# Optimization experiments

Measured on AMD Instinct MI355X. Metric: run time of the kernel, lower is better.

The kernel has to match this reference:

```python
import jax, jax.numpy as jnp
import numpy as np
import math

N, E, G = 20000, 160000, 256
H, L, R, LAT, TD = 128, 4, 64, 128, 64
CUT = 6.0
NTYPES = 101  # max_atomic_num=100 -> 101 rows, row 0 is padding


def _lin(key, fan_in, fan_out):
    kw, _ = jax.random.split(key)
    w = jax.random.normal(kw, (fan_in, fan_out), jnp.float32) / np.sqrt(fan_in).astype(np.float32)
    b = jnp.zeros((fan_out,), jnp.float32)
    return w, b


def _stack_lin(key, fan_in, fan_out):
    keys = jax.random.split(key, L)
    ws, bs = zip(*[_lin(k, fan_in, fan_out) for k in keys])
    return jnp.stack(ws), jnp.stack(bs)


def setup_inputs() -> dict:
    key = jax.random.key(0)
    ks = list(jax.random.split(key, 24))
    noisy_coords = jax.random.uniform(ks[0], (N, 3), jnp.float32)
    noisy_types = jax.random.randint(ks[1], (N,), 0, NTYPES)
    z = jax.random.normal(ks[2], (G, LAT), jnp.float32)
    t = jax.random.uniform(ks[3], (G,), jnp.float32) * 1000.0
    edge_index = jax.random.randint(ks[4], (2, E), 0, N)
    batch = jnp.sort(jax.random.randint(ks[5], (N,), 0, G))
    lattice = jnp.eye(3, dtype=jnp.float32)[None] * 5.0 + 0.1 * jax.random.normal(ks[6], (G, 3, 3), jnp.float32)
    offsets = jax.random.randint(ks[7], (E, 3), -1, 2).astype(jnp.float32)
    atom_embed = jax.random.normal(ks[8], (NTYPES, H), jnp.float32) * 0.02
    atom_embed = atom_embed.at[0].set(0.0)  # padding_idx=0
    z_w, z_b = _lin(ks[9], LAT, H)
    t_w, t_b = _lin(ks[10], TD, H)
    msg_w1, msg_b1 = _stack_lin(ks[11], H, H)
    msg_w2, msg_b2 = _stack_lin(ks[12], H, 3 * H)
    rbf_w, rbf_b = _stack_lin(ks[13], R, 3 * H)
    U = jax.random.normal(ks[14], (L, H, H), jnp.float32) / np.sqrt(H).astype(np.float32)
    V = jax.random.normal(ks[15], (L, H, H), jnp.float32) / np.sqrt(H).astype(np.float32)
    upd_w1, upd_b1 = _stack_lin(ks[16], 2 * H, H)
    upd_w2, upd_b2 = _stack_lin(ks[17], H, 3 * H)
    hc_w1, hc_b1 = _lin(ks[18], H, H)
    hc_w2, hc_b2 = _lin(ks[19], H, 3)
    ht_w1, ht_b1 = _lin(ks[20], H, H)
    ht_w2, ht_b2 = _lin(ks[21], H, NTYPES)
    return dict(noisy_coords=noisy_coords, noisy_types=noisy_types, z=z, t=t,
                edge_index=edge_index, batch=batch, lattice=lattice, offsets=offsets,
                atom_embed=atom_embed, z_w=z_w, z_b=z_b, t_w=t_w, t_b=t_b,
                msg_w1=msg_w1, msg_b1=msg_b1, msg_w2=msg_w2, msg_b2=msg_b2,
                rbf_w=rbf_w, rbf_b=rbf_b, U=U, V=V,
                upd_w1=upd_w1, upd_b1=upd_b1, upd_w2=upd_w2, upd_b2=upd_b2,
                hc_w1=hc_w1, hc_b1=hc_b1, hc_w2=hc_w2, hc_b2=hc_b2,
                ht_w1=ht_w1, ht_b1=ht_b1, ht_w2=ht_w2, ht_b2=ht_b2)


def reference(noisy_coords, noisy_types, z, t, edge_index, batch, lattice, offsets,
              atom_embed, z_w, z_b, t_w, t_b,
              msg_w1, msg_b1, msg_w2, msg_b2, rbf_w, rbf_b, U, V,
              upd_w1, upd_b1, upd_w2, upd_b2,
              hc_w1, hc_b1, hc_w2, hc_b2, ht_w1, ht_b1, ht_w2, ht_b2):
    n = noisy_coords.shape[0]
    src, dst = edge_index[0], edge_index[1]

    # node embeddings + conditioning
    s = atom_embed[noisy_types]                       # [N, H]
    v = jnp.zeros((n, 3, H), s.dtype)                 # [N, 3, H]
    half = TD // 2
    freqs = jnp.exp(-math.log(10000.0) * jnp.arange(half, dtype=jnp.float32) / (half - 1))
    emb = t[:, None] * freqs[None, :]                 # [G, TD/2]
    t_emb = jnp.concatenate([jnp.sin(emb), jnp.cos(emb)], axis=-1)  # [G, TD]
    cond = (z @ z_w + z_b)[batch] + (t_emb @ t_w + t_b)[batch]      # [N, H]

    # edge geometry: gather -> diff -> 3x3 matmul -> norm -> RBF -> normalize
    frac_diff = noisy_coords[dst] - noisy_coords[src] + offsets     # [E, 3]
    cart = jnp.einsum('ei,eij->ej', frac_diff, lattice[batch[src]]) # [E, 3]
    dist = jnp.maximum(jnp.sqrt(jnp.sum(cart * cart, -1)), 1e-8)    # clamp(min=1e-8)
    centers = jnp.linspace(0.0, CUT, R)
    gamma = jnp.float32(R / CUT)
    rbf = jnp.exp(-gamma * (dist[:, None] - centers[None, :]) ** 2) # [E, R]
    unit = cart / jnp.maximum(jnp.sqrt(jnp.sum(cart * cart, -1, keepdims=True)), 1e-12)

    # PaiNN layers (canonical message + update blocks)
    for l in range(L):
        s = s + cond
        # message block
        phi = jax.nn.silu(s @ msg_w1[l] + msg_b1[l]) @ msg_w2[l] + msg_b2[l]  # [N, 3H]
        filt = rbf @ rbf_w[l] + rbf_b[l]                                      # [E, 3H]
        x = phi[src] * filt
        ds, dv1, dv2 = jnp.split(x, 3, axis=-1)
        s = s + jax.ops.segment_sum(ds, dst, num_segments=n)
        vmsg = dv1[:, None, :] * v[src] + dv2[:, None, :] * unit[:, :, None]  # [E, 3, H]
        v = v + jax.ops.segment_sum(vmsg, dst, num_segments=n)
        # update block
        Uv = jnp.einsum('nch,hk->nck', v, U[l])
        Vv = jnp.einsum('nch,hk->nck', v, V[l])
        Vn = jnp.sqrt(jnp.sum(Vv * Vv, axis=1) + 1e-8)                        # [N, H]
        a = jax.nn.silu(jnp.concatenate([s, Vn], -1) @ upd_w1[l] + upd_b1[l]) @ upd_w2[l] + upd_b2[l]
        avv, asv, ass = jnp.split(a, 3, axis=-1)
        v = v + avv[:, None, :] * Uv
        s = s + asv * jnp.sum(Uv * Vv, axis=1) + ass

    coords_out = jax.nn.silu(s @ hc_w1 + hc_b1) @ hc_w2 + hc_b2   # [N, 3]
    type_out = jax.nn.silu(s @ ht_w1 + ht_b1) @ ht_w2 + ht_b2     # [N, 101]
    return coords_out, type_out
```

## Files before the change

kernel.cpp:

```cpp
#include <hip/hip_runtime.h>
#include <hip/hip_bf16.h>

#define HD 128
#define RD 64
#define H3 384

typedef float f32x4 __attribute__((ext_vector_type(4)));
typedef unsigned short us8 __attribute__((ext_vector_type(8)));
typedef __bf16 bf16x8 __attribute__((ext_vector_type(8)));

__device__ __forceinline__ float silu_f(float x) {
    return x / (1.0f + __expf(-x));
}
__device__ __forceinline__ unsigned short f2bf(float x) {
    __hip_bfloat16 h = __float2bfloat16(x);
    return *reinterpret_cast<unsigned short*>(&h);
}
__device__ __forceinline__ float bf2f(unsigned short u) {
    return __uint_as_float(((unsigned)u) << 16);
}
__device__ __forceinline__ f32x4 mfma3(us8 ah, us8 al, us8 bh, us8 bl, f32x4 c) {
    bf16x8 AH = __builtin_bit_cast(bf16x8, ah);
    bf16x8 AL = __builtin_bit_cast(bf16x8, al);
    bf16x8 BH = __builtin_bit_cast(bf16x8, bh);
    bf16x8 BL = __builtin_bit_cast(bf16x8, bl);
    c = __builtin_amdgcn_mfma_f32_16x16x32_bf16(AH, BH, c, 0, 0, 0);
    c = __builtin_amdgcn_mfma_f32_16x16x32_bf16(AH, BL, c, 0, 0, 0);
    c = __builtin_amdgcn_mfma_f32_16x16x32_bf16(AL, BH, c, 0, 0, 0);
    return c;
}

__global__ void wprep_kernel(const float* __restrict__ src,
                             unsigned short* __restrict__ dhi, unsigned short* __restrict__ dlo,
                             int K, int OUT, int sStride, int dStride, int nlay) {
    int total = K * OUT;
    for (int idx = blockIdx.x * blockDim.x + threadIdx.x; idx < total * nlay;
         idx += gridDim.x * blockDim.x) {
        int lyr = idx / total, r = idx % total;
        int o = r / K, k = r % K;
        float x = src[(size_t)lyr * sStride + (size_t)k * OUT + o];
        unsigned short hi = f2bf(x);
        unsigned short lo = f2bf(x - bf2f(hi));
        dhi[(size_t)lyr * dStride + (size_t)o * K + k] = hi;
        dlo[(size_t)lyr * dStride + (size_t)o * K + k] = lo;
    }
}

__global__ __launch_bounds__(128) void cond_kernel(const float* __restrict__ z, const float* __restrict__ t,
                            const float* __restrict__ z_w, const float* __restrict__ z_b,
                            const float* __restrict__ t_w, const float* __restrict__ t_b,
                            float* __restrict__ condG) {
    int g = blockIdx.x;
    int k = threadIdx.x;
    __shared__ float zr[128];
    __shared__ float te[64];
    zr[k] = z[g * 128 + k];
    if (k < 32) {
        float f = __expf(-9.2103403719761836f * (float)k / 31.0f);
        float e = t[g] * f;
        te[k] = sinf(e);
        te[32 + k] = cosf(e);
    }
    __syncthreads();
    float acc = z_b[k] + t_b[k];
    #pragma unroll 8
    for (int i = 0; i < 128; ++i) acc += zr[i] * z_w[i * 128 + k];
    #pragma unroll 8
    for (int i = 0; i < 64; ++i) acc += te[i] * t_w[i * 128 + k];
    condG[g * 128 + k] = acc;
}

__global__ void init_kernel(const int* __restrict__ types, const float* __restrict__ emb,
                            const float* __restrict__ condG, const int* __restrict__ batch,
                            float* __restrict__ s, int N_) {
    int i = blockIdx.x * blockDim.x + threadIdx.x;
    if (i < N_ * HD) {
        int n = i >> 7;
        int k = i & 127;
        s[i] = emb[types[n] * HD + k] + condG[batch[n] * 128 + k];
    }
}

__global__ void geom_kernel(const float* __restrict__ coords, const int* __restrict__ srcI,
                            const int* __restrict__ dstI, const int* __restrict__ batch,
                            const float* __restrict__ lattice, const float* __restrict__ offs,
                            float* __restrict__ dist, float* __restrict__ unit, int E_) {
    int e = blockIdx.x * blockDim.x + threadIdx.x;
    if (e >= E_) return;
    int sn = srcI[e], dn = dstI[e];
    float f0 = coords[dn * 3 + 0] - coords[sn * 3 + 0] + offs[e * 3 + 0];
    float f1 = coords[dn * 3 + 1] - coords[sn * 3 + 1] + offs[e * 3 + 1];
    float f2 = coords[dn * 3 + 2] - coords[sn * 3 + 2] + offs[e * 3 + 2];
    const float* Lg = lattice + batch[sn] * 9;
    float c0 = f0 * Lg[0] + f1 * Lg[3] + f2 * Lg[6];
    float c1 = f0 * Lg[1] + f1 * Lg[4] + f2 * Lg[7];
    float c2 = f0 * Lg[2] + f1 * Lg[5] + f2 * Lg[8];
    float nrm = sqrtf(c0 * c0 + c1 * c1 + c2 * c2);
    dist[e] = fmaxf(nrm, 1e-8f);
    float inv = 1.0f / fmaxf(nrm, 1e-12f);
    unit[e * 3 + 0] = c0 * inv;
    unit[e * 3 + 1] = c1 * inv;
    unit[e * 3 + 2] = c2 * inv;
}

__global__ void hist_kernel(const int* __restrict__ dstI, int* __restrict__ cnt, int E_) {
    int e = blockIdx.x * blockDim.x + threadIdx.x;
    if (e < E_) atomicAdd(&cnt[dstI[e]], 1);
}

__global__ __launch_bounds__(1024) void scan_kernel(const int* __restrict__ cnt, int* __restrict__ cur, int n) {
    __shared__ int tmp[1024];
    __shared__ int carry_s;
    if (threadIdx.x == 0) carry_s = 0;
    __syncthreads();
    for (int base = 0; base < n; base += 1024) {
        int i = base + threadIdx.x;
        int x = (i < n) ? cnt[i] : 0;
        tmp[threadIdx.x] = x;
        __syncthreads();
        for (int off = 1; off < 1024; off <<= 1) {
            int y = (threadIdx.x >= off) ? tmp[threadIdx.x - off] : 0;
            __syncthreads();
            tmp[threadIdx.x] += y;
            __syncthreads();
        }
        if (i < n) cur[i] = carry_s + tmp[threadIdx.x] - x;
        __syncthreads();
        if (threadIdx.x == 0) carry_s += tmp[1023];
        __syncthreads();
    }
}

__global__ void scatter_kernel(const int* __restrict__ srcI, const int* __restrict__ dstI,
                               const float* __restrict__ dist, const float* __restrict__ unit,
                               int* __restrict__ cur,
                               float* __restrict__ dist_s, float* __restrict__ unit_s,
                               int* __restrict__ src_s, int* __restrict__ dst_s, int E_) {
    int e = blockIdx.x * blockDim.x + threadIdx.x;
    if (e >= E_) return;
    int d = dstI[e];
    int p = atomicAdd(&cur[d], 1);
    dist_s[p] = dist[e];
    unit_s[p * 3 + 0] = unit[e * 3 + 0];
    unit_s[p * 3 + 1] = unit[e * 3 + 1];
    unit_s[p * 3 + 2] = unit[e * 3 + 2];
    src_s[p] = srcI[e];
    dst_s[p] = d;
}

#define PSA 136
__global__ __launch_bounds__(256, 2) void phi_mfma(
    const float* __restrict__ s,
    const unsigned short* __restrict__ w1h, const unsigned short* __restrict__ w1l,
    const float* __restrict__ b1,
    const unsigned short* __restrict__ w2h, const unsigned short* __restrict__ w2l,
    const float* __restrict__ b2,
    float* __restrict__ phi, int N_) {
    __shared__ unsigned short Ah[32 * PSA], Al[32 * PSA], Hh[32 * PSA], Hl[32 * PSA];
    const int tid = threadIdx.x;
    const int n0 = blockIdx.x * 32;
    for (int idx = tid; idx < 32 * 128; idx += 256) {
        int j = idx >> 7, k = idx & 127;
        int n = n0 + j; if (n >= N_) n = N_ - 1;
        float x = s[(size_t)n * 128 + k];
        unsigned short h = f2bf(x);
        Ah[j * PSA + k] = h;
        Al[j * PSA + k] = f2bf(x - bf2f(h));
    }
    __syncthreads();
    const int w = tid >> 6, l = tid & 63;
    const int lr = l & 15, lk = (l >> 4) << 3, rg0 = (l >> 4) << 2;
    const f32x4 zero4 = {0.0f, 0.0f, 0.0f, 0.0f};
    f32x4 acc1[2][2];
    #pragma unroll
    for (int rt = 0; rt < 2; ++rt)
        #pragma unroll
        for (int ci = 0; ci < 2; ++ci) acc1[rt][ci] = zero4;
    #pragma unroll
    for (int kt = 0; kt < 4; ++kt) {
        int kk = kt * 32 + lk;
        us8 bh[2], bl[2], ah[2], alo[2];
        #pragma unroll
        for (int ci = 0; ci < 2; ++ci) {
            int col = (w * 2 + ci) * 16 + lr;
            bh[ci] = *(const us8*)(w1h + (size_t)col * 128 + kk);
            bl[ci] = *(const us8*)(w1l + (size_t)col * 128 + kk);
        }
        #pragma unroll
        for (int rt = 0; rt < 2; ++rt) {
            ah[rt]  = *(const us8*)(Ah + (rt * 16 + lr) * PSA + kk);
            alo[rt] = *(const us8*)(Al + (rt * 16 + lr) * PSA + kk);
        }
        #pragma unroll
        for (int rt = 0; rt < 2; ++rt)
            #pragma unroll
            for (int ci = 0; ci < 2; ++ci)
                acc1[rt][ci] = mfma3(ah[rt], alo[rt], bh[ci], bl[ci], acc1[rt][ci]);
    }
    #pragma unroll
    for (int rt = 0; rt < 2; ++rt)
        #pragma unroll
        for (int ci = 0; ci < 2; ++ci) {
            int col = (w * 2 + ci) * 16 + lr;
            float bb = b1[col];
            #pragma unroll
            for (int rg = 0; rg < 4; ++rg) {
                int j = rt * 16 + rg0 + rg;
                float hv = silu_f(acc1[rt][ci][rg] + bb);
                unsigned short hh = f2bf(hv);
                Hh[j * PSA + col] = hh;
                Hl[j * PSA + col] = f2bf(hv - bf2f(hh));
            }
        }
    __syncthreads();
    f32x4 acc2[2][6];
    #pragma unroll
    for (int rt = 0; rt < 2; ++rt)
        #pragma unroll
        for (int ci = 0; ci < 6; ++ci) acc2[rt][ci] = zero4;
    #pragma unroll
    for (int kt = 0; kt < 4; ++kt) {
        int kk = kt * 32 + lk;
        us8 ah[2], alo[2];
        #pragma unroll
        for (int rt = 0; rt < 2; ++rt) {
            ah[rt]  = *(const us8*)(Hh + (rt * 16 + lr) * PSA + kk);
            alo[rt] = *(const us8*)(Hl + (rt * 16 + lr) * PSA + kk);
        }
        #pragma unroll
        for (int ci = 0; ci < 6; ++ci) {
            int col = (w * 6 + ci) * 16 + lr;
            us8 bh = *(const us8*)(w2h + (size_t)col * 128 + kk);
            us8 bl = *(const us8*)(w2l + (size_t)col * 128 + kk);
            #pragma unroll
            for (int rt = 0; rt < 2; ++rt)
                acc2[rt][ci] = mfma3(ah[rt], alo[rt], bh, bl, acc2[rt][ci]);
        }
    }
    #pragma unroll
    for (int rt = 0; rt < 2; ++rt)
        #pragma unroll
        for (int ci = 0; ci < 6; ++ci) {
            int col = (w * 6 + ci) * 16 + lr;
            float bb = b2[col];
            #pragma unroll
            for (int rg = 0; rg < 4; ++rg) {
                int j = rt * 16 + rg0 + rg;
                int n = n0 + j;
                if (n < N_) phi[(size_t)n * 384 + col] = acc2[rt][ci][rg] + bb;
            }
        }
}

__global__ __launch_bounds__(256, 2) void upd_mfma(
    const unsigned short* __restrict__ Uh, const unsigned short* __restrict__ Ul,
    const unsigned short* __restrict__ Vh, const unsigned short* __restrict__ Vl,
    const unsigned short* __restrict__ w1h, const unsigned short* __restrict__ w1l,
    const float* __restrict__ b1,
    const unsigned short* __restrict__ w2h, const unsigned short* __restrict__ w2l,
    const float* __restrict__ b2,
    float* __restrict__ s, float* __restrict__ v, const float* __restrict__ dv,
    const float* __restrict__ condG, const int* __restrict__ batch, int addcond, int N_) {
    __shared__ unsigned short SMA[2 * 48 * 136];
    __shared__ float UvL[48 * 132];
    __shared__ float VvL[48 * 132];
    unsigned short* VNh = SMA;
    unsigned short* VNl = SMA + 48 * 136;
    unsigned short* A1h = SMA;
    unsigned short* A1l = SMA + 16 * 264;
    unsigned short* a1h = SMA + 32 * 264;
    unsigned short* a1l = SMA + 32 * 264 + 16 * 136;
    float* o384 = VvL;
    const int tid = threadIdx.x;
    const int n0 = blockIdx.x * 16;
    for (int idx = tid; idx < 48 * 128; idx += 256) {
        int r = idx >> 7, k = idx & 127;
        int c = r >> 4, j = r & 15;
        int n = n0 + j; if (n >= N_) n = N_ - 1;
        size_t off = (size_t)n * 384 + c * 128 + k;
        float x = v[off] + dv[off];
        unsigned short h = f2bf(x);
        VNh[r * 136 + k] = h;
        VNl[r * 136 + k] = f2bf(x - bf2f(h));
    }
    __syncthreads();
    const int w = tid >> 6, l = tid & 63;
    const int lr = l & 15, lk = (l >> 4) << 3, rg0 = (l >> 4) << 2;
    const f32x4 zero4 = {0.0f, 0.0f, 0.0f, 0.0f};
    {
        f32x4 acc[3][2];
        #pragma unroll
        for (int rt = 0; rt < 3; ++rt) { acc[rt][0] = zero4; acc[rt][1] = zero4; }
        #pragma unroll
        for (int kt = 0; kt < 4; ++kt) {
            int kk = kt * 32 + lk;
            us8 bh[2], bl[2];
            #pragma unroll
            for (int ci = 0; ci < 2; ++ci) {
                int col = (w * 2 + ci) * 16 + lr;
                bh[ci] = *(const us8*)(Uh + (size_t)col * 128 + kk);
                bl[ci] = *(const us8*)(Ul + (size_t)col * 128 + kk);
            }
            #pragma unroll
            for (int rt = 0; rt < 3; ++rt) {
                us8 ah  = *(const us8*)(VNh + (rt * 16 + lr) * 136 + kk);
                us8 alo = *(const us8*)(VNl + (rt * 16 + lr) * 136 + kk);
                #pragma unroll
                for (int ci = 0; ci < 2; ++ci)
                    acc[rt][ci] = mfma3(ah, alo, bh[ci], bl[ci], acc[rt][ci]);
            }
        }
        #pragma unroll
        for (int rt = 0; rt < 3; ++rt)
            #pragma unroll
            for (int ci = 0; ci < 2; ++ci) {
                int col = (w * 2 + ci) * 16 + lr;
                #pragma unroll
                for (int rg = 0; rg < 4; ++rg)
                    UvL[(rt * 16 + rg0 + rg) * 132 + col] = acc[rt][ci][rg];
            }
        #pragma unroll
        for (int rt = 0; rt < 3; ++rt) { acc[rt][0] = zero4; acc[rt][1] = zero4; }
        #pragma unroll
        for (int kt = 0; kt < 4; ++kt) {
            int kk = kt * 32 + lk;
            us8 bh[2], bl[2];
            #pragma unroll
            for (int ci = 0; ci < 2; ++ci) {
                int col = (w * 2 + ci) * 16 + lr;
                bh[ci] = *(const us8*)(Vh + (size_t)col * 128 + kk);
                bl[ci] = *(const us8*)(Vl + (size_t)col * 128 + kk);
            }
            #pragma unroll
            for (int rt = 0; rt < 3; ++rt) {
                us8 ah  = *(const us8*)(VNh + (rt * 16 + lr) * 136 + kk);
                us8 alo = *(const us8*)(VNl + (rt * 16 + lr) * 136 + kk);
                #pragma unroll
                for (int ci = 0; ci < 2; ++ci)
                    acc[rt][ci] = mfma3(ah, alo, bh[ci], bl[ci], acc[rt][ci]);
            }
        }
        #pragma unroll
        for (int rt = 0; rt < 3; ++rt)
            #pragma unroll
            for (int ci = 0; ci < 2; ++ci) {
                int col = (w * 2 + ci) * 16 + lr;
                #pragma unroll
                for (int rg = 0; rg < 4; ++rg)
                    VvL[(rt * 16 + rg0 + rg) * 132 + col] = acc[rt][ci][rg];
            }
    }
    __syncthreads();
    float dotr[8];
    {
        int k = tid & 127;
        int jb = (tid >> 7) * 8;
        #pragma unroll
        for (int i = 0; i < 8; ++i) {
            int j = jb + i;
            float uv0 = UvL[j * 132 + k], uv1 = UvL[(16 + j) * 132 + k], uv2 = UvL[(32 + j) * 132 + k];
            float vv0 = VvL[j * 132 + k], vv1 = VvL[(16 + j) * 132 + k], vv2 = VvL[(32 + j) * 132 + k];
            dotr[i] = uv0 * vv0 + uv1 * vv1 + uv2 * vv2;
            float vnv = sqrtf(vv0 * vv0 + vv1 * vv1 + vv2 * vv2 + 1e-8f);
            int n = n0 + j; if (n >= N_) n = N_ - 1;
            float sv = s[(size_t)n * 128 + k];
            unsigned short h1 = f2bf(sv);
            A1h[j * 264 + k] = h1;
            A1l[j * 264 + k] = f2bf(sv - bf2f(h1));
            unsigned short h2 = f2bf(vnv);
            A1h[j * 264 + 128 + k] = h2;
            A1l[j * 264 + 128 + k] = f2bf(vnv - bf2f(h2));
        }
    }
    __syncthreads();
    {
        f32x4 acc[2]; acc[0] = zero4; acc[1] = zero4;
        #pragma unroll
        for (int kt = 0; kt < 8; ++kt) {
            int kk = kt * 32 + lk;
            us8 ah  = *(const us8*)(A1h + lr * 264 + kk);
            us8 alo = *(const us8*)(A1l + lr * 264 + kk);
            #pragma unroll
            for (int ci = 0; ci < 2; ++ci) {
                int col = (w * 2 + ci) * 16 + lr;
                us8 bh = *(const us8*)(w1h + (size_t)col * 256 + kk);
                us8 bl = *(const us8*)(w1l + (size_t)col * 256 + kk);
                acc[ci] = mfma3(ah, alo, bh, bl, acc[ci]);
            }
        }
        #pragma unroll
        for (int ci = 0; ci < 2; ++ci) {
            int col = (w * 2 + ci) * 16 + lr;
            float bb = b1[col];
            #pragma unroll
            for (int rg = 0; rg < 4; ++rg) {
                int j = rg0 + rg;
                float hv = silu_f(acc[ci][rg] + bb);
                unsigned short hh = f2bf(hv);
                a1h[j * 136 + col] = hh;
                a1l[j * 136 + col] = f2bf(hv - bf2f(hh));
            }
        }
    }
    __syncthreads();
    {
        f32x4 acc[6];
        #pragma unroll
        for (int ci = 0; ci < 6; ++ci) acc[ci] = zero4;
        #pragma unroll
        for (int kt = 0; kt < 4; ++kt) {
            int kk = kt * 32 + lk;
            us8 ah  = *(const us8*)(a1h + lr * 136 + kk);
            us8 alo = *(const us8*)(a1l + lr * 136 + kk);
            #pragma unroll
            for (int ci = 0; ci < 6; ++ci) {
                int col = (w * 6 + ci) * 16 + lr;
                us8 bh = *(const us8*)(w2h + (size_t)col * 128 + kk);
                us8 bl = *(const us8*)(w2l + (size_t)col * 128 + kk);
                acc[ci] = mfma3(ah, alo, bh, bl, acc[ci]);
            }
        }
        #pragma unroll
        for (int ci = 0; ci < 6; ++ci) {
            int col = (w * 6 + ci) * 16 + lr;
            float bb = b2[col];
            #pragma unroll
            for (int rg = 0; rg < 4; ++rg) {
                int j = rg0 + rg;
                o384[j * 388 + col] = acc[ci][rg] + bb;
            }
        }
    }
    __syncthreads();
    {
        int k = tid & 127;
        int jb = (tid >> 7) * 8;
        #pragma unroll
        for (int i = 0; i < 8; ++i) {
            int j = jb + i;
            int n = n0 + j;
            if (n >= N_) continue;
            float a0  = o384[j * 388 + k];
            float aH  = o384[j * 388 + 128 + k];
            float a2v = o384[j * 388 + 256 + k];
            #pragma unroll
            for (int c = 0; c < 3; ++c) {
                size_t off = (size_t)n * 384 + c * 128 + k;
                v[off] = v[off] + dv[off] + a0 * UvL[(c * 16 + j) * 132 + k];
            }
            float cadd = addcond ? condG[(size_t)batch[n] * 128 + k] : 0.0f;
            s[(size_t)n * 128 + k] += aH * dotr[i] + a2v + cadd;
        }
    }
}

#define EPB 128
__global__ __launch_bounds__(512) void edge_kernel(
    const float* __restrict__ phi, const float* __restrict__ v,
    const float* __restrict__ dist_s, const float* __restrict__ unit_s,
    const int* __restrict__ src_s, const int* __restrict__ dst_s,
    const float* __restrict__ rw, const float* __restrict__ rb,
    float* __restrict__ s, float* __restrict__ dv, int E_) {
    __shared__ unsigned short w_lds[RD * H3];
    __shared__ float rbf_lds[4][4][RD];
    for (int i = threadIdx.x; i < RD * H3; i += 512) {
        w_lds[i] = f2bf(rw[i]);
    }
    int sub = threadIdx.x >> 7;
    int col = threadIdx.x & 127;
    float b0 = rb[col], b1 = rb[128 + col], b2 = rb[256 + col];
    int span0 = blockIdx.x * EPB + sub * 32;
    float as = 0.0f, ad0 = 0.0f, ad1 = 0.0f, ad2 = 0.0f;
    int rd = -1;
    for (int it = 0; it < 8; ++it) {
        int eb = span0 + it * 4;
        __syncthreads();
        {
            int r = col & 63;
            int jbase = col >> 6;
            #pragma unroll
            for (int jj = 0; jj < 2; ++jj) {
                int j = jbase + 2 * jj;
                int e = eb + j;
                float val = 0.0f;
                if (e < E_) {
                    float d = dist_s[e];
                    float c = 6.0f * (float)r / 63.0f;
                    float tt = d - c;
                    val = __expf(-(64.0f / 6.0f) * tt * tt);
                }
                rbf_lds[sub][j][r] = val;
            }
        }
        __syncthreads();
        float f[4][3] = {};
        #pragma unroll 4
        for (int r = 0; r < 64; ++r) {
            float w0 = bf2f(w_lds[r * 384 + col]);
            float w1 = bf2f(w_lds[r * 384 + 128 + col]);
            float w2 = bf2f(w_lds[r * 384 + 256 + col]);
            #pragma unroll
            for (int j = 0; j < 4; ++j) {
                float rbv = rbf_lds[sub][j][r];
                f[j][0] += rbv * w0;
                f[j][1] += rbv * w1;
                f[j][2] += rbv * w2;
            }
        }
        #pragma unroll
        for (int j = 0; j < 4; ++j) {
            int e = eb + j;
            if (e >= E_) break;
            int dn = dst_s[e];
            if (dn != rd) {
                if (rd >= 0) {
                    atomicAdd(&s[(size_t)rd * 128 + col], as);
                    atomicAdd(&dv[(size_t)rd * 384 + col], ad0);
                    atomicAdd(&dv[(size_t)rd * 384 + 128 + col], ad1);
                    atomicAdd(&dv[(size_t)rd * 384 + 256 + col], ad2);
                }
                as = ad0 = ad1 = ad2 = 0.0f;
                rd = dn;
            }
            int sn = src_s[e];
            const float* phr = phi + (size_t)sn * 384;
            const float* vr = v + (size_t)sn * 384;
            float x0 = phr[col] * (f[j][0] + b0);
            float x1 = phr[128 + col] * (f[j][1] + b1);
            float x2 = phr[256 + col] * (f[j][2] + b2);
            float u0 = unit_s[e * 3 + 0], u1 = unit_s[e * 3 + 1], u2 = unit_s[e * 3 + 2];
            as += x0;
            ad0 += x1 * vr[col] + x2 * u0;
            ad1 += x1 * vr[128 + col] + x2 * u1;
            ad2 += x1 * vr[256 + col] + x2 * u2;
        }
    }
    if (rd >= 0) {
        atomicAdd(&s[(size_t)rd * 128 + col], as);
        atomicAdd(&dv[(size_t)rd * 384 + col], ad0);
        atomicAdd(&dv[(size_t)rd * 384 + 128 + col], ad1);
        atomicAdd(&dv[(size_t)rd * 384 + 256 + col], ad2);
    }
}

#define HPB 8
__global__ __launch_bounds__(128, 4) void heads_kernel(
    const float* __restrict__ s,
    const float* __restrict__ hc_w1, const float* __restrict__ hc_b1,
    const float* __restrict__ hc_w2, const float* __restrict__ hc_b2,
    const float* __restrict__ ht_w1, const float* __restrict__ ht_b1,
    const float* __restrict__ ht_w2, const float* __restrict__ ht_b2,
    float* __restrict__ outc, float* __restrict__ outt, int N_) {
    int n0 = blockIdx.x * HPB;
    int k = threadIdx.x;
    __shared__ float sr[HPB][128];
    __shared__ float h1[HPB][128];
    __shared__ float h2[HPB][128];
    #pragma unroll
    for (int j = 0; j < HPB; ++j) {
        int n = n0 + j;
        sr[j][k] = (n < N_) ? s[(size_t)n * 128 + k] : 0.0f;
    }
    __syncthreads();
    float a[HPB], b[HPB];
    #pragma unroll
    for (int j = 0; j < HPB; ++j) { a[j] = hc_b1[k]; b[j] = ht_b1[k]; }
    for (int h = 0; h < 128; h += 4) {
        float wa0 = hc_w1[h * 128 + k],       wa1 = hc_w1[(h + 1) * 128 + k];
        float wa2 = hc_w1[(h + 2) * 128 + k], wa3 = hc_w1[(h + 3) * 128 + k];
        float wb0 = ht_w1[h * 128 + k],       wb1 = ht_w1[(h + 1) * 128 + k];
        float wb2 = ht_w1[(h + 2) * 128 + k], wb3 = ht_w1[(h + 3) * 128 + k];
        #pragma unroll
        for (int j = 0; j < HPB; ++j) {
            const float4 x = *reinterpret_cast<const float4*>(&sr[j][h]);
            a[j] = fmaf(x.w, wa3, fmaf(x.z, wa2, fmaf(x.y, wa1, fmaf(x.x, wa0, a[j]))));
            b[j] = fmaf(x.w, wb3, fmaf(x.z, wb2, fmaf(x.y, wb1, fmaf(x.x, wb0, b[j]))));
        }
    }
    #pragma unroll
    for (int j = 0; j < HPB; ++j) {
        h1[j][k] = silu_f(a[j]);
        h2[j][k] = silu_f(b[j]);
    }
    __syncthreads();
    if (k < 101) {
        for (int j = 0; j < HPB; ++j) {
            int n = n0 + j;
            if (n >= N_) break;
            float c = ht_b2[k];
            #pragma unroll 4
            for (int h = 0; h < 128; ++h) c += h2[j][h] * ht_w2[h * 101 + k];
            outt[(size_t)n * 101 + k] = c;
        }
    }
    if (k < 3) {
        for (int j = 0; j < HPB; ++j) {
            int n = n0 + j;
            if (n >= N_) break;
            float c = hc_b2[k];
            #pragma unroll 4
            for (int h = 0; h < 128; ++h) c += h1[j][h] * hc_w2[h * 3 + k];
            outc[(size_t)n * 3 + k] = c;
        }
    }
}

extern "C" void kernel_launch(void* const* d_in, const int* in_sizes, int n_in,
                              void* d_out, int out_size, void* d_ws, size_t ws_size,
                              hipStream_t stream) {
    const float* coords  = (const float*)d_in[0];
    const int*   types   = (const int*)d_in[1];
    const float* z       = (const float*)d_in[2];
    const float* t       = (const float*)d_in[3];
    const int*   eidx    = (const int*)d_in[4];
    const int*   batch   = (const int*)d_in[5];
    const float* lattice = (const float*)d_in[6];
    const float* offs    = (const float*)d_in[7];
    const float* aemb    = (const float*)d_in[8];
    const float* z_w     = (const float*)d_in[9];
    const float* z_b     = (const float*)d_in[10];
    const float* t_w     = (const float*)d_in[11];
    const float* t_b     = (const float*)d_in[12];
    const float* msg_w1  = (const float*)d_in[13];
    const float* msg_b1  = (const float*)d_in[14];
    const float* msg_w2  = (const float*)d_in[15];
    const float* msg_b2  = (const float*)d_in[16];
    const float* rbf_w   = (const float*)d_in[17];
    const float* rbf_b   = (const float*)d_in[18];
    const float* Um      = (const float*)d_in[19];
    const float* Vm      = (const float*)d_in[20];
    const float* upd_w1  = (const float*)d_in[21];
    const float* upd_b1  = (const float*)d_in[22];
    const float* upd_w2  = (const float*)d_in[23];
    const float* upd_b2  = (const float*)d_in[24];
    const float* hc_w1   = (const float*)d_in[25];
    const float* hc_b1   = (const float*)d_in[26];
    const float* hc_w2   = (const float*)d_in[27];
    const float* hc_b2   = (const float*)d_in[28];
    const float* ht_w1   = (const float*)d_in[29];
    const float* ht_b1   = (const float*)d_in[30];
    const float* ht_w2   = (const float*)d_in[31];
    const float* ht_b2   = (const float*)d_in[32];

    const int N = in_sizes[1];
    const int G = in_sizes[3];
    const int E = in_sizes[4] / 2;
    const int* srcI = eidx;
    const int* dstI = eidx + E;

    char* ws = (char*)d_ws;
    auto alloc = [&](size_t bytes) {
        char* p = ws;
        ws += (bytes + 255) & ~(size_t)255;
        return p;
    };
    float* s_buf   = (float*)alloc((size_t)N * HD * 4);
    float* v_buf   = (float*)alloc((size_t)N * H3 * 4);
    float* dv_buf  = (float*)alloc((size_t)N * H3 * 4);
    float* phi_buf = (float*)alloc((size_t)N * H3 * 4);
    float* condG   = (float*)alloc((size_t)G * HD * 4);
    float* dist_s  = (float*)alloc((size_t)E * 4);
    float* unit_s  = (float*)alloc((size_t)E * 3 * 4);
    int*   src_s   = (int*)alloc((size_t)E * 4);
    int*   dst_s   = (int*)alloc((size_t)E * 4);
    int*   cur     = (int*)alloc((size_t)N * 4);
    unsigned short* wpr = (unsigned short*)alloc((size_t)4 * 360448 * 2);
    const size_t LS = 360448;
    float* dist_t  = phi_buf;
    float* unit_t  = phi_buf + E;

    hipMemsetAsync(v_buf, 0, (size_t)N * H3 * 4, stream);
    hipMemsetAsync(cur, 0, (size_t)N * 4, stream);
    cond_kernel<<<G, 128, 0, stream>>>(z, t, z_w, z_b, t_w, t_b, condG);
    init_kernel<<<(N * HD + 255) / 256, 256, 0, stream>>>(types, aemb, condG, batch, s_buf, N);
    geom_kernel<<<(E + 255) / 256, 256, 0, stream>>>(coords, srcI, dstI, batch, lattice, offs, dist_t, unit_t, E);
    hist_kernel<<<(E + 255) / 256, 256, 0, stream>>>(dstI, cur, E);
    {
        int* cnt2 = (int*)(phi_buf + 4 * (size_t)E);
        hipMemcpyAsync(cnt2, cur, (size_t)N * 4, hipMemcpyDeviceToDevice, stream);
        scan_kernel<<<1, 1024, 0, stream>>>(cnt2, cur, N);
    }
    scatter_kernel<<<(E + 255) / 256, 256, 0, stream>>>(srcI, dstI, dist_t, unit_t, cur,
                                                        dist_s, unit_s, src_s, dst_s, E);
    wprep_kernel<<<256, 256, 0, stream>>>(msg_w1, wpr + 0,      wpr + 16384,  128, 128, 16384, (int)LS, 4);
    wprep_kernel<<<768, 256, 0, stream>>>(msg_w2, wpr + 32768,  wpr + 81920,  128, 384, 49152, (int)LS, 4);
    wprep_kernel<<<512, 256, 0, stream>>>(upd_w1, wpr + 131072, wpr + 163840, 256, 128, 32768, (int)LS, 4);
    wprep_kernel<<<768, 256, 0, stream>>>(upd_w2, wpr + 196608, wpr + 245760, 128, 384, 49152, (int)LS, 4);
    wprep_kernel<<<256, 256, 0, stream>>>(Um,     wpr + 294912, wpr + 311296, 128, 128, 16384, (int)LS, 4);
    wprep_kernel<<<256, 256, 0, stream>>>(Vm,     wpr + 327680, wpr + 344064, 128, 128, 16384, (int)LS, 4);

    int eblocks = (E + EPB - 1) / EPB;
    int pblocks = (N + 31) / 32;
    int ublocks = (N + 15) / 16;
    int hblocks = (N + HPB - 1) / HPB;
    for (int l = 0; l < 4; ++l) {
        const unsigned short* L = wpr + (size_t)l * LS;
        phi_mfma<<<pblocks, 256, 0, stream>>>(s_buf,
                L + 0, L + 16384, msg_b1 + (size_t)l * HD,
                L + 32768, L + 81920, msg_b2 + (size_t)l * H3,
                phi_buf, N);
        hipMemsetAsync(dv_buf, 0, (size_t)N * H3 * 4, stream);
        edge_kernel<<<eblocks, 512, 0, stream>>>(phi_buf, v_buf, dist_s, unit_s, src_s, dst_s,
                                                 rbf_w + (size_t)l * RD * H3, rbf_b + (size_t)l * H3,
                                                 s_buf, dv_buf, E);
        upd_mfma<<<ublocks, 256, 0, stream>>>(
                L + 294912, L + 311296, L + 327680, L + 344064,
                L + 131072, L + 163840, upd_b1 + (size_t)l * HD,
                L + 196608, L + 245760, upd_b2 + (size_t)l * H3,
                s_buf, v_buf, dv_buf, condG, batch, (l < 3) ? 1 : 0, N);
    }
    heads_kernel<<<hblocks, 128, 0, stream>>>(s_buf, hc_w1, hc_b1, hc_w2, hc_b2,
                                        ht_w1, ht_b1, ht_w2, ht_b2,
                                        (float*)d_out, (float*)d_out + (size_t)N * 3, N);
}
```

Baseline: 1.465 ms.

## Compute edge RBF filter with split-bf16 MFMA using prepacked weights

Replaces the scalar FMA loop that computed the per-edge RBF filter (64x384 weights held as bf16 in LDS) with split-bf16 (hi/lo) MFMA tiles over 64-edge blocks. The filter is staged through LDS for the existing scatter/atomic accumulation. The RBF weights are now pre-split into hi/lo bf16 once per launch by wprep, which removes the per-block conversion of the 24K-element weight matrix into LDS. The new kernel uses 256-thread blocks with a large LDS footprint (about 68KB), which may limit occupancy. It also halves edges per block, so more atomic flushes happen at block boundaries.

```diff
diff --git a/kernel.cpp b/kernel.cpp
--- a/kernel.cpp
+++ b/kernel.cpp
@@ -454,62 +454,84 @@
     }
 }
 
-#define EPB 128
-__global__ __launch_bounds__(512) void edge_kernel(
+#define EB 64
+__global__ __launch_bounds__(256, 2) void edge_mfma(
     const float* __restrict__ phi, const float* __restrict__ v,
     const float* __restrict__ dist_s, const float* __restrict__ unit_s,
     const int* __restrict__ src_s, const int* __restrict__ dst_s,
-    const float* __restrict__ rw, const float* __restrict__ rb,
+    const unsigned short* __restrict__ rwh, const unsigned short* __restrict__ rwl,
+    const float* __restrict__ rb,
     float* __restrict__ s, float* __restrict__ dv, int E_) {
-    __shared__ unsigned short w_lds[RD * H3];
-    __shared__ float rbf_lds[4][4][RD];
-    for (int i = threadIdx.x; i < RD * H3; i += 512) {
-        w_lds[i] = f2bf(rw[i]);
-    }
-    int sub = threadIdx.x >> 7;
-    int col = threadIdx.x & 127;
+    __shared__ unsigned short Rh[64 * 72];
+    __shared__ unsigned short Rl[64 * 72];
+    __shared__ float filt[32 * 388];
+    const int tid = threadIdx.x;
+    const int e0 = blockIdx.x * EB;
+    #pragma unroll
+    for (int i = 0; i < 16; ++i) {
+        int idx = i * 256 + tid;
+        int e = idx >> 6, r = idx & 63;
+        float val = 0.0f;
+        int ge = e0 + e;
+        if (ge < E_) {
+            float d = dist_s[ge];
+            float c = 6.0f * (float)r / 63.0f;
+            float tt = d - c;
+            val = __expf(-(64.0f / 6.0f) * tt * tt);
+        }
+        unsigned short h = f2bf(val);
+        Rh[e * 72 + r] = h;
+        Rl[e * 72 + r] = f2bf(val - bf2f(h));
+    }
+    __syncthreads();
+    const int w = tid >> 6, l = tid & 63;
+    const int lr = l & 15, lk = (l >> 4) << 3, rg0 = (l >> 4) << 2;
+    const f32x4 zero4 = {0.0f, 0.0f, 0.0f, 0.0f};
+    f32x4 acc[4][6];
+    #pragma unroll
+    for (int mt = 0; mt < 4; ++mt)
+        #pragma unroll
+        for (int nt = 0; nt < 6; ++nt) acc[mt][nt] = zero4;
+    #pragma unroll
+    for (int kt = 0; kt < 2; ++kt) {
+        int kk = kt * 32 + lk;
+        us8 ah[4], al[4];
+        #pragma unroll
+        for (int mt = 0; mt < 4; ++mt) {
+            ah[mt] = *(const us8*)(Rh + (mt * 16 + lr) * 72 + kk);
+            al[mt] = *(const us8*)(Rl + (mt * 16 + lr) * 72 + kk);
+        }
+        #pragma unroll
+        for (int nt = 0; nt < 6; ++nt) {
+            int col = w * 96 + nt * 16 + lr;
+            us8 bh = *(const us8*)(rwh + (size_t)col * 64 + kk);
+            us8 bl = *(const us8*)(rwl + (size_t)col * 64 + kk);
+            #pragma unroll
+            for (int mt = 0; mt < 4; ++mt)
+                acc[mt][nt] = mfma3(ah[mt], al[mt], bh, bl, acc[mt][nt]);
+        }
+    }
+    const int sub = tid >> 7;
+    const int col = tid & 127;
     float b0 = rb[col], b1 = rb[128 + col], b2 = rb[256 + col];
-    int span0 = blockIdx.x * EPB + sub * 32;
     float as = 0.0f, ad0 = 0.0f, ad1 = 0.0f, ad2 = 0.0f;
     int rd = -1;
-    for (int it = 0; it < 8; ++it) {
-        int eb = span0 + it * 4;
+    #pragma unroll
+    for (int ch = 0; ch < 2; ++ch) {
         __syncthreads();
-        {
-            int r = col & 63;
-            int jbase = col >> 6;
-            #pragma unroll
-            for (int jj = 0; jj < 2; ++jj) {
-                int j = jbase + 2 * jj;
-                int e = eb + j;
-                float val = 0.0f;
-                if (e < E_) {
-                    float d = dist_s[e];
-                    float c = 6.0f * (float)r / 63.0f;
-                    float tt = d - c;
-                    val = __expf(-(64.0f / 6.0f) * tt * tt);
-                }
-                rbf_lds[sub][j][r] = val;
-            }
-        }
+        #pragma unroll
+        for (int mt = 0; mt < 2; ++mt)
+            #pragma unroll
+            for (int nt = 0; nt < 6; ++nt) {
+                int c2 = w * 96 + nt * 16 + lr;
+                #pragma unroll
+                for (int rg = 0; rg < 4; ++rg)
+                    filt[(mt * 16 + rg0 + rg) * 388 + c2] = acc[2 * ch + mt][nt][rg];
+            }
         __syncthreads();
-        float f[4][3] = {};
-        #pragma unroll 4
-        for (int r = 0; r < 64; ++r) {
-            float w0 = bf2f(w_lds[r * 384 + col]);
-            float w1 = bf2f(w_lds[r * 384 + 128 + col]);
-            float w2 = bf2f(w_lds[r * 384 + 256 + col]);
-            #pragma unroll
-            for (int j = 0; j < 4; ++j) {
-                float rbv = rbf_lds[sub][j][r];
-                f[j][0] += rbv * w0;
-                f[j][1] += rbv * w1;
-                f[j][2] += rbv * w2;
-            }
-        }
-        #pragma unroll
-        for (int j = 0; j < 4; ++j) {
-            int e = eb + j;
+        int le0 = ch * 32 + sub * 16;
+        for (int i = 0; i < 16; ++i) {
+            int e = e0 + le0 + i;
             if (e >= E_) break;
             int dn = dst_s[e];
             if (dn != rd) {
@@ -523,11 +545,15 @@
                 rd = dn;
             }
             int sn = src_s[e];
+            int fr = sub * 16 + i;
+            float f0 = filt[fr * 388 + col] + b0;
+            float f1 = filt[fr * 388 + 128 + col] + b1;
+            float f2v = filt[fr * 388 + 256 + col] + b2;
             const float* phr = phi + (size_t)sn * 384;
             const float* vr = v + (size_t)sn * 384;
-            float x0 = phr[col] * (f[j][0] + b0);
-            float x1 = phr[128 + col] * (f[j][1] + b1);
-            float x2 = phr[256 + col] * (f[j][2] + b2);
+            float x0 = phr[col] * f0;
+            float x1 = phr[128 + col] * f1;
+            float x2 = phr[256 + col] * f2v;
             float u0 = unit_s[e * 3 + 0], u1 = unit_s[e * 3 + 1], u2 = unit_s[e * 3 + 2];
             as += x0;
             ad0 += x1 * vr[col] + x2 * u0;
@@ -664,8 +690,8 @@
     int*   src_s   = (int*)alloc((size_t)E * 4);
     int*   dst_s   = (int*)alloc((size_t)E * 4);
     int*   cur     = (int*)alloc((size_t)N * 4);
-    unsigned short* wpr = (unsigned short*)alloc((size_t)4 * 360448 * 2);
-    const size_t LS = 360448;
+    const size_t LS = 409600;
+    unsigned short* wpr = (unsigned short*)alloc((size_t)4 * LS * 2);
     float* dist_t  = phi_buf;
     float* unit_t  = phi_buf + E;
 
@@ -688,8 +714,9 @@
     wprep_kernel<<<768, 256, 0, stream>>>(upd_w2, wpr + 196608, wpr + 245760, 128, 384, 49152, (int)LS, 4);
     wprep_kernel<<<256, 256, 0, stream>>>(Um,     wpr + 294912, wpr + 311296, 128, 128, 16384, (int)LS, 4);
     wprep_kernel<<<256, 256, 0, stream>>>(Vm,     wpr + 327680, wpr + 344064, 128, 128, 16384, (int)LS, 4);
-
-    int eblocks = (E + EPB - 1) / EPB;
+    wprep_kernel<<<384, 256, 0, stream>>>(rbf_w,  wpr + 360448, wpr + 385024, 64,  384, 24576, (int)LS, 4);
+
+    int eblocks = (E + EB - 1) / EB;
     int pblocks = (N + 31) / 32;
     int ublocks = (N + 15) / 16;
     int hblocks = (N + HPB - 1) / HPB;
@@ -700,9 +727,10 @@
                 L + 32768, L + 81920, msg_b2 + (size_t)l * H3,
                 phi_buf, N);
         hipMemsetAsync(dv_buf, 0, (size_t)N * H3 * 4, stream);
-        edge_kernel<<<eblocks, 512, 0, stream>>>(phi_buf, v_buf, dist_s, unit_s, src_s, dst_s,
-                                                 rbf_w + (size_t)l * RD * H3, rbf_b + (size_t)l * H3,
-                                                 s_buf, dv_buf, E);
+        edge_mfma<<<eblocks, 256, 0, stream>>>(phi_buf, v_buf, dist_s, unit_s, src_s, dst_s,
+                                               L + 360448, L + 385024,
+                                               rbf_b + (size_t)l * H3,
+                                               s_buf, dv_buf, E);
         upd_mfma<<<ublocks, 256, 0, stream>>>(
                 L + 294912, L + 311296, L + 327680, L + 344064,
                 L + 131072, L + 163840, upd_b1 + (size_t)l * HD,
```

Result: slower. 1.625 ms (+10.9%).
